# Performance work log

Measured on AMD Instinct MI355X. Metric: run time of the kernel, lower is better.

## Reference

```python
import jax, jax.numpy as jnp
import numpy as np

D_MODEL = 1024
N_HEADS = 16
D_HEAD = D_MODEL // N_HEADS


def setup_inputs() -> dict:
    key = jax.random.key(0)
    ks = jax.random.split(key, 6)
    query = jax.random.normal(ks[0], (2, 2048, D_MODEL), dtype=jnp.float32)
    context = jax.random.normal(ks[1], (2, 4096, D_MODEL), dtype=jnp.float32)
    s = 1.0 / np.sqrt(D_MODEL)
    Wq = jax.random.normal(ks[2], (D_MODEL, D_MODEL), dtype=jnp.float32) * s
    Wk = jax.random.normal(ks[3], (D_MODEL, D_MODEL), dtype=jnp.float32) * s
    Wv = jax.random.normal(ks[4], (D_MODEL, D_MODEL), dtype=jnp.float32) * s
    Wo = jax.random.normal(ks[5], (D_MODEL, D_MODEL), dtype=jnp.float32) * s
    return {"query": query, "context": context, "Wq": Wq, "Wk": Wk, "Wv": Wv, "Wo": Wo}


def reference(query, context, Wq, Wk, Wv, Wo):
    B, T_q, D = query.shape
    T_c = context.shape[1]
    # nn.Linear(bias=False): y = x @ W.T
    Q = (query @ Wq.T).reshape(B, T_q, N_HEADS, D_HEAD)
    K = (context @ Wk.T).reshape(B, T_c, N_HEADS, D_HEAD)
    V = (context @ Wv.T).reshape(B, T_c, N_HEADS, D_HEAD)
    scale = jnp.sqrt(jnp.asarray(D_HEAD, dtype=query.dtype))
    # non-causal cross-attention; chunking in the original is mathematically
    # identical to the full softmax attention below
    scores = jnp.einsum('bqhd,bkhd->bhqk', Q, K) / scale
    attn = jax.nn.softmax(scores, axis=-1)
    out = jnp.einsum('bhqk,bkhd->bqhd', attn, V).reshape(B, T_q, D)
    return out @ Wo.T
```

## Files before the change

kernel.cpp:

```cpp
#include <hip/hip_runtime.h>

typedef __attribute__((__ext_vector_type__(4))) float f32x4;
typedef __attribute__((__ext_vector_type__(16))) float f32x16;
typedef __attribute__((__ext_vector_type__(8))) __bf16 bf16x8;
typedef __attribute__((__ext_vector_type__(8))) unsigned short u16x8;
typedef __attribute__((__ext_vector_type__(4))) unsigned int u32x4;

#define AS1 __attribute__((address_space(1)))
#define AS3 __attribute__((address_space(3)))

#define SC 0.18033688011112042f
#define MSC 5.7707801635558535f

__device__ __forceinline__ unsigned short f2bf(float f) {
  unsigned int u = __float_as_uint(f);
  u += 0x7FFFu + ((u >> 16) & 1u);
  return (unsigned short)(u >> 16);
}
__device__ __forceinline__ float bf2f(unsigned short u) {
  return __uint_as_float((unsigned int)u << 16);
}
__device__ __forceinline__ unsigned int packtrunc(float lo, float hi) {
  return (__float_as_uint(hi) & 0xFFFF0000u) | (__float_as_uint(lo) >> 16);
}

__global__ void cast_all(const float* __restrict__ q, const float* __restrict__ c,
                         const float* __restrict__ wq, const float* __restrict__ wk,
                         const float* __restrict__ wv, const float* __restrict__ wo,
                         unsigned short* __restrict__ qb, unsigned short* __restrict__ cb,
                         unsigned short* __restrict__ wqb, unsigned short* __restrict__ wkb,
                         unsigned short* __restrict__ wvb, unsigned short* __restrict__ wob) {
  const int blk = blockIdx.x;
  const float* s; unsigned short* d; int off;
  if (blk < 4096)        { s = q;  d = qb;  off = blk; }
  else if (blk < 12288)  { s = c;  d = cb;  off = blk - 4096; }
  else if (blk < 13312)  { s = wq; d = wqb; off = blk - 12288; }
  else if (blk < 14336)  { s = wk; d = wkb; off = blk - 13312; }
  else if (blk < 15360)  { s = wv; d = wvb; off = blk - 14336; }
  else                   { s = wo; d = wob; off = blk - 15360; }
  const long i = ((long)off * 256 + threadIdx.x) * 4;
  float4 v = *reinterpret_cast<const float4*>(s + i);
  ushort4 o;
  o.x = f2bf(v.x); o.y = f2bf(v.y); o.z = f2bf(v.z); o.w = f2bf(v.w);
  *reinterpret_cast<ushort4*>(d + i) = o;
}

__device__ __forceinline__ void gemm_core(const unsigned short* __restrict__ A,
                                          const unsigned short* __restrict__ Bt,
                                          unsigned short* As, unsigned short* Bs,
                                          int m0, int n0, f32x4 acc[4][2]) {
  const int tid = threadIdx.x, lane = tid & 63, wid = tid >> 6;
  const int fr = lane & 15, fg = lane >> 4;
  const int wr = wid >> 2, wc = wid & 3;
  const int srow = tid >> 2;
  const int scol = (tid & 3) * 8;
  const unsigned short* a0 = A + (long)(m0 + srow) * 1024 + scol;
  const unsigned short* b0 = Bt + (long)(n0 + srow) * 1024 + scol;

  for (int k0 = 0; k0 < 1024; k0 += 32) {
    __builtin_amdgcn_global_load_lds((const AS1 void*)(a0 + k0),
                                     (AS3 void*)(As + wid * 512), 16, 0, 0);
    __builtin_amdgcn_global_load_lds((const AS1 void*)(b0 + k0),
                                     (AS3 void*)(Bs + wid * 512), 16, 0, 0);
    __syncthreads();
    bf16x8 af[4], bfr[2];
#pragma unroll
    for (int m = 0; m < 4; ++m)
      af[m] = *reinterpret_cast<const bf16x8*>(&As[(wr * 64 + m * 16 + fr) * 32 + fg * 8]);
#pragma unroll
    for (int n = 0; n < 2; ++n)
      bfr[n] = *reinterpret_cast<const bf16x8*>(&Bs[(wc * 32 + n * 16 + fr) * 32 + fg * 8]);
#pragma unroll
    for (int m = 0; m < 4; ++m)
#pragma unroll
      for (int n = 0; n < 2; ++n)
        acc[m][n] = __builtin_amdgcn_mfma_f32_16x16x32_bf16(af[m], bfr[n], acc[m][n], 0, 0, 0);
    __syncthreads();
  }
}

__global__ __launch_bounds__(512) void proj_fused(const unsigned short* __restrict__ qb,
                                                  const unsigned short* __restrict__ cb,
                                                  const unsigned short* __restrict__ wqb,
                                                  const unsigned short* __restrict__ wkb,
                                                  const unsigned short* __restrict__ wvb,
                                                  unsigned short* __restrict__ Qb,
                                                  unsigned short* __restrict__ Kb,
                                                  unsigned short* __restrict__ Vt) {
  const int raw = blockIdx.x;
  const int bid = (raw & 7) * 160 + (raw >> 3);
  const unsigned short *A, *Bt; unsigned short* C; int mode, loc;
  float oscale = 1.0f;
  if (bid < 256)      { A = qb; Bt = wqb; C = Qb; mode = 0; loc = bid; oscale = SC; }
  else if (bid < 768) { A = cb; Bt = wkb; C = Kb; mode = 0; loc = bid - 256; }
  else                { A = cb; Bt = wvb; C = Vt; mode = 2; loc = bid - 768; }
  const int m0 = (loc >> 3) << 7, n0 = (loc & 7) << 7;

  __shared__ __align__(16) unsigned short As[128 * 32];
  __shared__ __align__(16) unsigned short Bs[128 * 32];
  f32x4 acc[4][2];
#pragma unroll
  for (int m = 0; m < 4; ++m)
#pragma unroll
    for (int n = 0; n < 2; ++n) acc[m][n] = {0.f, 0.f, 0.f, 0.f};

  gemm_core(A, Bt, As, Bs, m0, n0, acc);

  const int lane = threadIdx.x & 63, wid = threadIdx.x >> 6;
  const int fr = lane & 15, fg = lane >> 4, wr = wid >> 2, wc = wid & 3;
  if (mode == 0) {
#pragma unroll
    for (int m = 0; m < 4; ++m) {
      const int row = m0 + wr * 64 + m * 16 + fg * 4;
#pragma unroll
      for (int n = 0; n < 2; ++n) {
        const int col = n0 + wc * 32 + n * 16 + fr;
#pragma unroll
        for (int r = 0; r < 4; ++r)
          C[(long)(row + r) * 1024 + col] = f2bf(acc[m][n][r] * oscale);
      }
    }
  } else {
#pragma unroll
    for (int m = 0; m < 4; ++m) {
      const int row = m0 + wr * 64 + m * 16 + fg * 4;
      const int bb = row >> 12, t = row & 4095;
#pragma unroll
      for (int n = 0; n < 2; ++n) {
        const int col = n0 + wc * 32 + n * 16 + fr;
        ushort4 o;
        o.x = f2bf(acc[m][n][0]); o.y = f2bf(acc[m][n][1]);
        o.z = f2bf(acc[m][n][2]); o.w = f2bf(acc[m][n][3]);
        *reinterpret_cast<ushort4*>(&C[((long)(bb * 1024 + col)) * 4096 + t]) = o;
      }
    }
  }
}

__global__ __launch_bounds__(512) void gemm_o(const unsigned short* __restrict__ A,
                                              const unsigned short* __restrict__ Bt,
                                              float* __restrict__ C) {
  const int raw = blockIdx.x;
  const int bid = (raw & 7) * 64 + (raw >> 3);
  const int m0 = (bid >> 4) << 7;
  const int n0 = (bid & 15) << 6;
  __shared__ __align__(16) unsigned short As[128 * 32];
  __shared__ __align__(16) unsigned short Bs[64 * 32];
  const int tid = threadIdx.x, lane = tid & 63, wid = tid >> 6;
  const int fr = lane & 15, fg = lane >> 4;
  const int wr = wid >> 2, wc = wid & 3;
  const int srow = tid >> 2;
  const int scol = (tid & 3) * 8;
  const unsigned short* a0 = A + (long)(m0 + srow) * 1024 + scol;
  const unsigned short* b0 = Bt + (long)(n0 + srow) * 1024 + scol;

  f32x4 acc[4];
#pragma unroll
  for (int m = 0; m < 4; ++m) acc[m] = {0.f, 0.f, 0.f, 0.f};

  for (int k0 = 0; k0 < 1024; k0 += 32) {
    __builtin_amdgcn_global_load_lds((const AS1 void*)(a0 + k0),
                                     (AS3 void*)(As + wid * 512), 16, 0, 0);
    if (wid < 4)
      __builtin_amdgcn_global_load_lds((const AS1 void*)(b0 + k0),
                                       (AS3 void*)(Bs + wid * 512), 16, 0, 0);
    __syncthreads();
    bf16x8 af[4], bfr;
#pragma unroll
    for (int m = 0; m < 4; ++m)
      af[m] = *reinterpret_cast<const bf16x8*>(&As[(wr * 64 + m * 16 + fr) * 32 + fg * 8]);
    bfr = *reinterpret_cast<const bf16x8*>(&Bs[(wc * 16 + fr) * 32 + fg * 8]);
#pragma unroll
    for (int m = 0; m < 4; ++m)
      acc[m] = __builtin_amdgcn_mfma_f32_16x16x32_bf16(af[m], bfr, acc[m], 0, 0, 0);
    __syncthreads();
  }

#pragma unroll
  for (int m = 0; m < 4; ++m) {
    const int row = m0 + wr * 64 + m * 16 + fg * 4;
    const int col = n0 + wc * 16 + fr;
#pragma unroll
    for (int r = 0; r < 4; ++r)
      C[(long)(row + r) * 1024 + col] = acc[m][r];
  }
}

__global__ __launch_bounds__(512, 4) void flash_attn(const unsigned short* __restrict__ Q,
                                                     const unsigned short* __restrict__ Kb,
                                                     const unsigned short* __restrict__ Vt,
                                                     unsigned short* __restrict__ Op,
                                                     float* __restrict__ Lp) {
  const int tid = threadIdx.x, lane = tid & 63, wid = tid >> 6;
  const int raw = (int)blockIdx.x;
  const int blk = (raw & 7) * 64 + (raw >> 3);
  const int kvh = blk & 1;
  const int qt = (blk >> 1) & 7;
  const int h = (blk >> 4) & 15;
  const int b = blk >> 8;
  const int q0 = qt * 256;
  const int l = lane & 31, hi = lane >> 5, l7 = l & 7;

  __shared__ __align__(16) unsigned short Ks[2][4096];
  __shared__ __align__(16) unsigned short Vs[2][4096];

  bf16x8 qf[4];
#pragma unroll
  for (int dk = 0; dk < 4; ++dk)
    qf[dk] = *reinterpret_cast<const bf16x8*>(
        &Q[(long)(b * 2048 + q0 + wid * 32 + l) * 1024 + h * 64 + dk * 16 + hi * 8]);

  f32x16 oacc[2];
  oacc[0] = (f32x16)(0.f); oacc[1] = (f32x16)(0.f);
  float lsum = 0.f;

  const int lr = lane >> 3;
  const int c8 = lane & 7;
  const unsigned short* ksrc =
      Kb + (long)(b * 4096 + kvh * 2048 + wid * 8 + lr) * 1024 + h * 64 + c8 * 8;
  const unsigned short* vsrc =
      Vt + (long)((b * 16 + h) * 64 + wid * 8 + lr) * 4096 + kvh * 2048 + c8 * 8;
  const int wk0 = (wid * 8 + lr) * 64 + ((c8 ^ lr) * 8);

  u16x8 rk0 = *reinterpret_cast<const u16x8*>(ksrc);
  u16x8 rv0 = *reinterpret_cast<const u16x8*>(vsrc);
  *reinterpret_cast<u16x8*>(&Ks[0][wk0]) = rk0;
  *reinterpret_cast<u16x8*>(&Vs[0][wk0]) = rv0;
  __syncthreads();

  for (int t = 0; t < 32; ++t) {
    const int cur = t & 1;
    if (t < 31) {
      rk0 = *reinterpret_cast<const u16x8*>(ksrc + (long)(t + 1) * 65536);
      rv0 = *reinterpret_cast<const u16x8*>(vsrc + (t + 1) * 64);
    }

    f32x16 s2[2];
    s2[0] = (f32x16)(-MSC); s2[1] = (f32x16)(-MSC);
#pragma unroll
    for (int kvb = 0; kvb < 2; ++kvb) {
#pragma unroll
      for (int dk = 0; dk < 4; ++dk) {
        const int r = kvb * 32 + l;
        bf16x8 kf = *reinterpret_cast<const bf16x8*>(
            &Ks[cur][r * 64 + (((dk * 2 + hi) ^ l7) * 8)]);
        s2[kvb] = __builtin_amdgcn_mfma_f32_32x32x16_bf16(kf, qf[dk], s2[kvb], 0, 0, 0);
      }
    }

    bf16x8 pA[4];
#pragma unroll
    for (int kvb = 0; kvb < 2; ++kvb) {
      float p[16];
      float ps = 0.f;
#pragma unroll
      for (int r = 0; r < 16; ++r) {
        p[r] = __builtin_amdgcn_exp2f(s2[kvb][r]);
        ps += p[r];
      }
      lsum += ps;
      unsigned int pk[8];
#pragma unroll
      for (int i = 0; i < 8; ++i) pk[i] = packtrunc(p[2 * i], p[2 * i + 1]);
      asm("v_permlane32_swap_b32 %0, %1" : "+v"(pk[0]), "+v"(pk[2]));
      asm("v_permlane32_swap_b32 %0, %1" : "+v"(pk[1]), "+v"(pk[3]));
      asm("v_permlane32_swap_b32 %0, %1" : "+v"(pk[4]), "+v"(pk[6]));
      asm("v_permlane32_swap_b32 %0, %1" : "+v"(pk[5]), "+v"(pk[7]));
      u32x4 w0 = {pk[0], pk[1], pk[2], pk[3]};
      u32x4 w1 = {pk[4], pk[5], pk[6], pk[7]};
      pA[kvb * 2] = __builtin_bit_cast(bf16x8, w0);
      pA[kvb * 2 + 1] = __builtin_bit_cast(bf16x8, w1);
    }

#pragma unroll
    for (int dblk = 0; dblk < 2; ++dblk) {
      const int r = dblk * 32 + l;
#pragma unroll
      for (int seg = 0; seg < 4; ++seg) {
        bf16x8 vf = *reinterpret_cast<const bf16x8*>(
            &Vs[cur][r * 64 + (((seg * 2 + hi) ^ l7) * 8)]);
        oacc[dblk] = __builtin_amdgcn_mfma_f32_32x32x16_bf16(pA[seg], vf, oacc[dblk], 0, 0, 0);
      }
    }

    if (t < 31) {
      *reinterpret_cast<u16x8*>(&Ks[cur ^ 1][wk0]) = rk0;
      *reinterpret_cast<u16x8*>(&Vs[cur ^ 1][wk0]) = rv0;
      __syncthreads();
    }
  }

  lsum += __shfl_xor(lsum, 32);
  const float inv = 1.0f / lsum;
  if (hi == 0)
    Lp[kvh * 65536 + (b * 2048 + q0 + wid * 32 + l) * 16 + h] = lsum;
  unsigned short* Oh = Op + (long)kvh * 4194304;
#pragma unroll
  for (int reg = 0; reg < 16; ++reg) {
    const int qrow = (reg & 3) + 8 * (reg >> 2) + 4 * hi;
    const float ivr = __shfl(inv, qrow, 64);
    const long rbase = (long)(b * 2048 + q0 + wid * 32 + qrow) * 1024 + h * 64;
    Oh[rbase + l] = f2bf(oacc[0][reg] * ivr);
    Oh[rbase + 32 + l] = f2bf(oacc[1][reg] * ivr);
  }
}

__global__ void combine(const unsigned short* __restrict__ Op,
                        const float* __restrict__ Lp,
                        unsigned short* __restrict__ AO) {
  const long i = ((long)blockIdx.x * 256 + threadIdx.x) * 8;
  const int row = (int)(i >> 10);
  const int h = ((int)(i >> 6)) & 15;
  const float l0 = Lp[row * 16 + h];
  const float l1 = Lp[65536 + row * 16 + h];
  const float inv = 1.0f / (l0 + l1);
  const float w0 = l0 * inv, w1 = l1 * inv;
  u16x8 a = *reinterpret_cast<const u16x8*>(Op + i);
  u16x8 bq = *reinterpret_cast<const u16x8*>(Op + 4194304 + i);
  u16x8 o;
#pragma unroll
  for (int j = 0; j < 8; ++j)
    o[j] = f2bf(bf2f(a[j]) * w0 + bf2f(bq[j]) * w1);
  *reinterpret_cast<u16x8*>(AO + i) = o;
}

extern "C" void kernel_launch(void* const* d_in, const int* in_sizes, int n_in,
                              void* d_out, int out_size, void* d_ws, size_t ws_size,
                              hipStream_t stream) {
  const float* query = (const float*)d_in[0];
  const float* context = (const float*)d_in[1];
  const float* Wq = (const float*)d_in[2];
  const float* Wk = (const float*)d_in[3];
  const float* Wv = (const float*)d_in[4];
  const float* Wo = (const float*)d_in[5];

  char* ws = (char*)d_ws;
  unsigned short* qb = (unsigned short*)(ws);
  unsigned short* cb = (unsigned short*)(ws + 8388608);
  unsigned short* wqb = (unsigned short*)(ws + 25165824);
  unsigned short* wkb = (unsigned short*)(ws + 27262976);
  unsigned short* wvb = (unsigned short*)(ws + 29360128);
  unsigned short* wob = (unsigned short*)(ws + 31457280);
  unsigned short* Qb = (unsigned short*)(ws + 33554432);
  unsigned short* Kb = (unsigned short*)(ws + 41943040);
  unsigned short* Vt = (unsigned short*)(ws + 58720256);
  unsigned short* Op = (unsigned short*)(ws + 8388608);
  float* Lp = (float*)(ws + 25165824);
  unsigned short* AO = qb;

  cast_all<<<16384, 256, 0, stream>>>(query, context, Wq, Wk, Wv, Wo,
                                      qb, cb, wqb, wkb, wvb, wob);
  proj_fused<<<1280, 512, 0, stream>>>(qb, cb, wqb, wkb, wvb, Qb, Kb, Vt);
  flash_attn<<<512, 512, 0, stream>>>(Qb, Kb, Vt, Op, Lp);
  combine<<<2048, 256, 0, stream>>>(Op, Lp, AO);
  gemm_o<<<512, 512, 0, stream>>>(AO, wob, (float*)d_out);
}
```

Baseline: 176.1 us.

## Split Q projection and fuse K/V projections sharing the context tile

Replaces the single fused projection kernel with a separate Q projection kernel and a K/V kernel. In the K/V kernel each block loads one context A-tile and multiplies it against both Wk and Wv tiles, so context reads are halved and there are more MFMAs per barrier. The cost is an extra kernel launch, twice the accumulator registers, more LDS per block, and fewer blocks (512) in the K/V grid, which may lower occupancy.

```diff
diff --git a/kernel.cpp b/kernel.cpp
--- a/kernel.cpp
+++ b/kernel.cpp
@@ -45,10 +45,14 @@
   *reinterpret_cast<ushort4*>(d + i) = o;
 }
 
-__device__ __forceinline__ void gemm_core(const unsigned short* __restrict__ A,
-                                          const unsigned short* __restrict__ Bt,
-                                          unsigned short* As, unsigned short* Bs,
-                                          int m0, int n0, f32x4 acc[4][2]) {
+__global__ __launch_bounds__(512) void proj_q(const unsigned short* __restrict__ A,
+                                              const unsigned short* __restrict__ Bt,
+                                              unsigned short* __restrict__ C) {
+  const int raw = blockIdx.x;
+  const int bid = (raw & 7) * 32 + (raw >> 3);
+  const int m0 = (bid >> 3) << 7, n0 = (bid & 7) << 7;
+  __shared__ __align__(16) unsigned short As[128 * 32];
+  __shared__ __align__(16) unsigned short Bs[128 * 32];
   const int tid = threadIdx.x, lane = tid & 63, wid = tid >> 6;
   const int fr = lane & 15, fg = lane >> 4;
   const int wr = wid >> 2, wc = wid & 3;
@@ -57,6 +61,12 @@
   const unsigned short* a0 = A + (long)(m0 + srow) * 1024 + scol;
   const unsigned short* b0 = Bt + (long)(n0 + srow) * 1024 + scol;
 
+  f32x4 acc[4][2];
+#pragma unroll
+  for (int m = 0; m < 4; ++m)
+#pragma unroll
+    for (int n = 0; n < 2; ++n) acc[m][n] = {0.f, 0.f, 0.f, 0.f};
+
   for (int k0 = 0; k0 < 1024; k0 += 32) {
     __builtin_amdgcn_global_load_lds((const AS1 void*)(a0 + k0),
                                      (AS3 void*)(As + wid * 512), 16, 0, 0);
@@ -77,62 +87,98 @@
         acc[m][n] = __builtin_amdgcn_mfma_f32_16x16x32_bf16(af[m], bfr[n], acc[m][n], 0, 0, 0);
     __syncthreads();
   }
-}
-
-__global__ __launch_bounds__(512) void proj_fused(const unsigned short* __restrict__ qb,
-                                                  const unsigned short* __restrict__ cb,
-                                                  const unsigned short* __restrict__ wqb,
-                                                  const unsigned short* __restrict__ wkb,
-                                                  const unsigned short* __restrict__ wvb,
-                                                  unsigned short* __restrict__ Qb,
-                                                  unsigned short* __restrict__ Kb,
-                                                  unsigned short* __restrict__ Vt) {
+
+#pragma unroll
+  for (int m = 0; m < 4; ++m) {
+    const int row = m0 + wr * 64 + m * 16 + fg * 4;
+#pragma unroll
+    for (int n = 0; n < 2; ++n) {
+      const int col = n0 + wc * 32 + n * 16 + fr;
+#pragma unroll
+      for (int r = 0; r < 4; ++r)
+        C[(long)(row + r) * 1024 + col] = f2bf(acc[m][n][r] * SC);
+    }
+  }
+}
+
+__global__ __launch_bounds__(512) void proj_kv(const unsigned short* __restrict__ cb,
+                                               const unsigned short* __restrict__ wkb,
+                                               const unsigned short* __restrict__ wvb,
+                                               unsigned short* __restrict__ Kb,
+                                               unsigned short* __restrict__ Vt) {
   const int raw = blockIdx.x;
-  const int bid = (raw & 7) * 160 + (raw >> 3);
-  const unsigned short *A, *Bt; unsigned short* C; int mode, loc;
-  float oscale = 1.0f;
-  if (bid < 256)      { A = qb; Bt = wqb; C = Qb; mode = 0; loc = bid; oscale = SC; }
-  else if (bid < 768) { A = cb; Bt = wkb; C = Kb; mode = 0; loc = bid - 256; }
-  else                { A = cb; Bt = wvb; C = Vt; mode = 2; loc = bid - 768; }
-  const int m0 = (loc >> 3) << 7, n0 = (loc & 7) << 7;
-
+  const int bid = (raw & 7) * 64 + (raw >> 3);
+  const int m0 = (bid >> 3) << 7, n0 = (bid & 7) << 7;
   __shared__ __align__(16) unsigned short As[128 * 32];
-  __shared__ __align__(16) unsigned short Bs[128 * 32];
-  f32x4 acc[4][2];
+  __shared__ __align__(16) unsigned short BsK[128 * 32];
+  __shared__ __align__(16) unsigned short BsV[128 * 32];
+  const int tid = threadIdx.x, lane = tid & 63, wid = tid >> 6;
+  const int fr = lane & 15, fg = lane >> 4;
+  const int wr = wid >> 2, wc = wid & 3;
+  const int srow = tid >> 2;
+  const int scol = (tid & 3) * 8;
+  const unsigned short* a0 = cb + (long)(m0 + srow) * 1024 + scol;
+  const unsigned short* bk0 = wkb + (long)(n0 + srow) * 1024 + scol;
+  const unsigned short* bv0 = wvb + (long)(n0 + srow) * 1024 + scol;
+
+  f32x4 aK[4][2], aV[4][2];
 #pragma unroll
   for (int m = 0; m < 4; ++m)
 #pragma unroll
-    for (int n = 0; n < 2; ++n) acc[m][n] = {0.f, 0.f, 0.f, 0.f};
-
-  gemm_core(A, Bt, As, Bs, m0, n0, acc);
-
-  const int lane = threadIdx.x & 63, wid = threadIdx.x >> 6;
-  const int fr = lane & 15, fg = lane >> 4, wr = wid >> 2, wc = wid & 3;
-  if (mode == 0) {
-#pragma unroll
-    for (int m = 0; m < 4; ++m) {
-      const int row = m0 + wr * 64 + m * 16 + fg * 4;
+    for (int n = 0; n < 2; ++n) {
+      aK[m][n] = {0.f, 0.f, 0.f, 0.f};
+      aV[m][n] = {0.f, 0.f, 0.f, 0.f};
+    }
+
+  for (int k0 = 0; k0 < 1024; k0 += 32) {
+    __builtin_amdgcn_global_load_lds((const AS1 void*)(a0 + k0),
+                                     (AS3 void*)(As + wid * 512), 16, 0, 0);
+    __builtin_amdgcn_global_load_lds((const AS1 void*)(bk0 + k0),
+                                     (AS3 void*)(BsK + wid * 512), 16, 0, 0);
+    __builtin_amdgcn_global_load_lds((const AS1 void*)(bv0 + k0),
+                                     (AS3 void*)(BsV + wid * 512), 16, 0, 0);
+    __syncthreads();
+    bf16x8 af[4], bK[2], bV[2];
+#pragma unroll
+    for (int m = 0; m < 4; ++m)
+      af[m] = *reinterpret_cast<const bf16x8*>(&As[(wr * 64 + m * 16 + fr) * 32 + fg * 8]);
+#pragma unroll
+    for (int n = 0; n < 2; ++n) {
+      bK[n] = *reinterpret_cast<const bf16x8*>(&BsK[(wc * 32 + n * 16 + fr) * 32 + fg * 8]);
+      bV[n] = *reinterpret_cast<const bf16x8*>(&BsV[(wc * 32 + n * 16 + fr) * 32 + fg * 8]);
+    }
+#pragma unroll
+    for (int m = 0; m < 4; ++m)
 #pragma unroll
       for (int n = 0; n < 2; ++n) {
-        const int col = n0 + wc * 32 + n * 16 + fr;
-#pragma unroll
-        for (int r = 0; r < 4; ++r)
-          C[(long)(row + r) * 1024 + col] = f2bf(acc[m][n][r] * oscale);
+        aK[m][n] = __builtin_amdgcn_mfma_f32_16x16x32_bf16(af[m], bK[n], aK[m][n], 0, 0, 0);
+        aV[m][n] = __builtin_amdgcn_mfma_f32_16x16x32_bf16(af[m], bV[n], aV[m][n], 0, 0, 0);
       }
-    }
-  } else {
-#pragma unroll
-    for (int m = 0; m < 4; ++m) {
-      const int row = m0 + wr * 64 + m * 16 + fg * 4;
-      const int bb = row >> 12, t = row & 4095;
-#pragma unroll
-      for (int n = 0; n < 2; ++n) {
-        const int col = n0 + wc * 32 + n * 16 + fr;
-        ushort4 o;
-        o.x = f2bf(acc[m][n][0]); o.y = f2bf(acc[m][n][1]);
-        o.z = f2bf(acc[m][n][2]); o.w = f2bf(acc[m][n][3]);
-        *reinterpret_cast<ushort4*>(&C[((long)(bb * 1024 + col)) * 4096 + t]) = o;
-      }
+    __syncthreads();
+  }
+
+#pragma unroll
+  for (int m = 0; m < 4; ++m) {
+    const int row = m0 + wr * 64 + m * 16 + fg * 4;
+#pragma unroll
+    for (int n = 0; n < 2; ++n) {
+      const int col = n0 + wc * 32 + n * 16 + fr;
+#pragma unroll
+      for (int r = 0; r < 4; ++r)
+        Kb[(long)(row + r) * 1024 + col] = f2bf(aK[m][n][r]);
+    }
+  }
+#pragma unroll
+  for (int m = 0; m < 4; ++m) {
+    const int row = m0 + wr * 64 + m * 16 + fg * 4;
+    const int bb = row >> 12, t = row & 4095;
+#pragma unroll
+    for (int n = 0; n < 2; ++n) {
+      const int col = n0 + wc * 32 + n * 16 + fr;
+      ushort4 o;
+      o.x = f2bf(aV[m][n][0]); o.y = f2bf(aV[m][n][1]);
+      o.z = f2bf(aV[m][n][2]); o.w = f2bf(aV[m][n][3]);
+      *reinterpret_cast<ushort4*>(&Vt[((long)(bb * 1024 + col)) * 4096 + t]) = o;
     }
   }
 }
@@ -350,7 +396,8 @@
 
   cast_all<<<16384, 256, 0, stream>>>(query, context, Wq, Wk, Wv, Wo,
                                       qb, cb, wqb, wkb, wvb, wob);
-  proj_fused<<<1280, 512, 0, stream>>>(qb, cb, wqb, wkb, wvb, Qb, Kb, Vt);
+  proj_q<<<256, 512, 0, stream>>>(qb, wqb, Qb);
+  proj_kv<<<512, 512, 0, stream>>>(cb, wkb, wvb, Kb, Vt);
   flash_attn<<<512, 512, 0, stream>>>(Qb, Kb, Vt, Op, Lp);
   combine<<<2048, 256, 0, stream>>>(Op, Lp, AO);
   gemm_o<<<512, 512, 0, stream>>>(AO, wob, (float*)d_out);
```

Result: slower. 180.6 us (+2.6%).
